# Optimization experiments

Measured on AMD Instinct MI355X. Metric: run time of the kernel, lower is better.

The kernel has to match this reference:

```python
import jax, jax.numpy as jnp
import numpy as np

B, S, F_IN, F_OUT = 8, 128, 768, 768
NUM_REL = 41           # num_dependencies + 1
NUM_LAYER = 2
N_HEAD, HID = 8, 96    # hidden_dim = embed_dim // n_head
EMB = 768


def setup_inputs() -> dict:
    key = jax.random.key(0)
    ks = jax.random.split(key, 14)
    s = 1.0 / np.sqrt(F_IN)
    inp = {
        "x": jax.random.normal(ks[0], (B, S, F_IN), dtype=jnp.float32),
        "adj": jax.random.uniform(ks[1], (B, NUM_REL, S, S), dtype=jnp.float32),
        "q": jax.random.normal(ks[2], (B, EMB), dtype=jnp.float32),
        # R-GCN params (stacked over layers)
        "w_rgcn": jax.random.uniform(ks[3], (NUM_LAYER, NUM_REL, F_IN, F_OUT), minval=-s, maxval=s),
        "score_w": jax.random.uniform(ks[4], (NUM_LAYER, F_OUT), minval=-s, maxval=s),
        "score_b": jax.random.uniform(ks[5], (NUM_LAYER,), minval=-s, maxval=s),
        # Attention params (stored as [in, out] for x @ W)
        "wk": jax.random.uniform(ks[6], (EMB, N_HEAD * HID), minval=-s, maxval=s),
        "bk": jnp.zeros((N_HEAD * HID,), jnp.float32),
        "wq": jax.random.uniform(ks[7], (EMB, N_HEAD * HID), minval=-s, maxval=s),
        "bq": jnp.zeros((N_HEAD * HID,), jnp.float32),
        "wbil": jax.random.uniform(ks[8], (HID, HID), minval=-1.0 / np.sqrt(HID), maxval=1.0 / np.sqrt(HID)),
        "wproj": jax.random.uniform(ks[9], (N_HEAD * HID, EMB), minval=-s, maxval=s),
        "bproj": jnp.zeros((EMB,), jnp.float32),
    }
    return inp


def _rgcn_layer(h, adj, w, sw, sb):
    # h: [B,S,I]; adj: [B,R,S,S]; w: [R,I,O]
    hidden = jnp.einsum("bsi,rio->brso", h, w)            # per-relation transform
    denom = jnp.sum(adj, axis=3, keepdims=True)           # [B,R,S,1]
    intm = jnp.einsum("brsk,brko->brso", adj, hidden)     # relation-wise aggregation
    div = intm / jnp.where(denom == 0, jnp.ones_like(denom), denom)
    logits = jnp.einsum("brso,o->brs", div, sw) + sb      # score Linear(out->1)
    r_coeffs = jax.nn.softmax(logits, axis=1)             # softmax over relations
    out = jnp.einsum("brso,brs->bso", div, r_coeffs)
    return jax.nn.relu(out)


def _attention(k, q, wk, bk, wq, bq, wbil, wproj, bproj):
    # k: [B,S,E]; q: [B,E] -> [B,1,E]
    q3 = q[:, None, :]
    kx = (k @ wk + bk).reshape(B, S, N_HEAD, HID)
    qx = (q3 @ wq + bq).reshape(B, 1, N_HEAD, HID)
    qw = jnp.einsum("bqhd,de->bqhe", qx, wbil)            # bi_linear score
    score = jnp.einsum("bqhe,bkhe->bhqk", qw, kx)
    attn = jax.nn.softmax(score, axis=-1)
    o = jnp.einsum("bhqk,bkhd->bqhd", attn, kx).reshape(B, 1, N_HEAD * HID)
    return o @ wproj + bproj                              # [B,1,EMB]


def reference(x, adj, q, w_rgcn, score_w, score_b, wk, bk, wq, bq, wbil, wproj, bproj):
    h = x
    for l in range(NUM_LAYER):
        h = _rgcn_layer(h, adj, w_rgcn[l], score_w[l], score_b[l])
    return _attention(h, q, wk, bk, wq, bq, wbil, wproj, bproj)
```

## Files before the change

### kernel.cpp

```cpp
#include <hip/hip_runtime.h>
#include <stdint.h>

#define B_ 8
#define S_ 128
#define R_ 41
#define F_ 768
#define NH_ 8
#define HID_ 96
#define BS_ (B_*S_)
#define SM_SCALE 256.0f

typedef _Float16 f16;
typedef _Float16 f16x8 __attribute__((ext_vector_type(8)));
typedef _Float16 f16x4 __attribute__((ext_vector_type(4)));
typedef float f32x4 __attribute__((ext_vector_type(4)));

#define GLD16(gp, lp) __builtin_amdgcn_global_load_lds((const __attribute__((address_space(1))) uint32_t*)(gp), (__attribute__((address_space(3))) uint32_t*)(lp), 16, 0, 0)

__device__ __forceinline__ float wredsum(float v){
  #pragma unroll
  for (int o=32;o;o>>=1) v += __shfl_down(v,o,64);
  return v;
}

__global__ __launch_bounds__(256) void kConvWV(const float* __restrict__ w, const float* __restrict__ sw,
                                               f16* __restrict__ wT, float* __restrict__ v) {
  int bid = blockIdx.x;
  int it = bid % 12, r = bid / 12;
  __shared__ float t[64*68];
  int tid = threadIdx.x;
  int ri = tid >> 2, c = tid & 3;
  float vacc = 0.f;
  for (int ot = 0; ot < 12; ++ot) {
    const float* src = w + ((size_t)r*F_ + (it*64 + ri))*F_ + ot*64 + c*16;
    const float* swp = sw + ot*64 + c*16;
    __syncthreads();
    #pragma unroll
    for (int j=0;j<4;j++){
      f32x4 v4 = *(const f32x4*)(src + j*4);
      f32x4 s4 = *(const f32x4*)(swp + j*4);
      vacc += v4.x*s4.x + v4.y*s4.y + v4.z*s4.z + v4.w*s4.w;
      *(f32x4*)&t[ri*68 + c*16 + j*4] = v4;
    }
    __syncthreads();
    int ro = tid >> 2;
    f16 outv[16];
    #pragma unroll
    for (int j=0;j<16;j++) outv[j] = (f16)t[(c*16+j)*68 + ro];
    f16* dst = wT + ((size_t)r*F_ + (ot*64+ro))*F_ + it*64 + c*16;
    *(f16x8*)dst = *(f16x8*)&outv[0];
    *(f16x8*)(dst+8) = *(f16x8*)&outv[8];
  }
  vacc += __shfl_down(vacc, 1, 64);
  vacc += __shfl_down(vacc, 2, 64);
  if (c == 0) v[(size_t)r*F_ + it*64 + ri] = vacc;
}

__global__ __launch_bounds__(256) void kConvW(const float* __restrict__ w, f16* __restrict__ wT) {
  int bid = blockIdx.x;
  int ot = bid % 12; int it = (bid/12) % 12; int r = bid / 144;
  __shared__ float t[64*68];
  int tid = threadIdx.x;
  int ri = tid >> 2, c = tid & 3;
  const float* src = w + ((size_t)r*F_ + (it*64 + ri))*F_ + ot*64 + c*16;
  #pragma unroll
  for (int j=0;j<4;j++){
    f32x4 v4 = *(const f32x4*)(src + j*4);
    *(f32x4*)&t[ri*68 + c*16 + j*4] = v4;
  }
  __syncthreads();
  int ro = tid >> 2;
  f16 outv[16];
  #pragma unroll
  for (int j=0;j<16;j++) outv[j] = (f16)t[(c*16+j)*68 + ro];
  f16* dst = wT + ((size_t)r*F_ + (ot*64+ro))*F_ + it*64 + c*16;
  *(f16x8*)dst = *(f16x8*)&outv[0];
  *(f16x8*)(dst+8) = *(f16x8*)&outv[8];
}

template<typename T>
__global__ __launch_bounds__(256) void kTransTo16T(const T* __restrict__ h, f16* __restrict__ hT) {
  int bid = blockIdx.x;
  int st = bid & 1; int ft = (bid>>1) % 12; int b = bid / 24;
  __shared__ f16 t[64*72];
  int tid = threadIdx.x;
  int sl = tid>>2, c = tid&3;
  const T* src = h + ((size_t)b*S_ + st*64 + sl)*F_ + ft*64 + c*16;
  f16 tmp[16];
  #pragma unroll
  for (int j=0;j<16;j++) tmp[j] = (f16)src[j];
  *(f16x8*)&t[sl*72 + c*16]     = *(f16x8*)&tmp[0];
  *(f16x8*)&t[sl*72 + c*16 + 8] = *(f16x8*)&tmp[8];
  __syncthreads();
  int fl = tid>>2;
  f16 outv[16];
  #pragma unroll
  for (int j=0;j<16;j++) outv[j] = t[(c*16+j)*72 + fl];
  f16* dst = hT + ((size_t)b*F_ + ft*64 + fl)*S_ + st*64 + c*16;
  *(f16x8*)dst = *(f16x8*)&outv[0];
  *(f16x8*)(dst+8) = *(f16x8*)&outv[8];
}

__global__ __launch_bounds__(256) void kU(const float* __restrict__ h, const float* __restrict__ v, float* __restrict__ u) {
  int idx = blockIdx.x*4 + (threadIdx.x>>6);
  int lane = threadIdx.x&63;
  int k = idx & 127;
  int br = idx >> 7;
  int r = br % R_;
  int b = br / R_;
  const float* hr = h + ((size_t)b*S_ + k)*F_ + lane*12;
  const float* vr = v + (size_t)r*F_ + lane*12;
  float acc=0.f;
  #pragma unroll
  for (int j=0;j<3;j++){
    f32x4 a = *(const f32x4*)(hr+j*4);
    f32x4 c4 = *(const f32x4*)(vr+j*4);
    acc += a.x*c4.x+a.y*c4.y+a.z*c4.z+a.w*c4.w;
  }
  acc = wredsum(acc);
  if (lane==0) u[idx] = acc;
}

__global__ __launch_bounds__(256) void kLogits(const float* __restrict__ adj, const float* __restrict__ u,
                        const float* __restrict__ sb_all, int l,
                        float* __restrict__ dinv, float* __restrict__ lg) {
  int idx = blockIdx.x*4 + (threadIdx.x>>6);
  int lane = threadIdx.x&63;
  const float* arow = adj + (size_t)idx*S_;
  int br = idx >> 7;
  const float* up = u + (size_t)br*S_;
  float a0 = arow[lane], a1 = arow[lane+64];
  float u0 = up[lane],   u1 = up[lane+64];
  float ssum = a0+a1;
  float sdot = a0*u0 + a1*u1;
  ssum = wredsum(ssum);
  sdot = wredsum(sdot);
  if (lane==0){
    float dv = (ssum==0.0f) ? 1.0f : (1.0f/ssum);
    dinv[idx] = dv;
    lg[idx] = sdot*dv + sb_all[l];
  }
}

__global__ __launch_bounds__(256) void kSoftmaxR(const float* __restrict__ lg, float* __restrict__ c) {
  int t = blockIdx.x*256 + threadIdx.x;
  int b = t >> 7, s = t & 127;
  float vals[R_];
  float mx = -1e30f;
  #pragma unroll
  for (int r=0;r<R_;r++){ float x = lg[((size_t)b*R_+r)*S_ + s]; vals[r]=x; mx = fmaxf(mx,x); }
  float sum=0.f;
  #pragma unroll
  for (int r=0;r<R_;r++){ vals[r] = expf(vals[r]-mx); sum += vals[r]; }
  float inv = 1.0f/sum;
  #pragma unroll
  for (int r=0;r<R_;r++) c[((size_t)b*R_+r)*S_+s] = vals[r]*inv;
}

__global__ __launch_bounds__(256) void kM16(const float* __restrict__ adj, const float* __restrict__ c,
                     const float* __restrict__ dinv, f16* __restrict__ M) {
  int t = blockIdx.x*256 + threadIdx.x;
  int brs = t >> 5; int k4 = (t & 31) * 4;
  float a = SM_SCALE * c[brs] * dinv[brs];
  f32x4 v4 = *(const f32x4*)(adj + (size_t)brs*S_ + k4);
  f16x4 o;
  o[0]=(f16)(v4.x*a); o[1]=(f16)(v4.y*a); o[2]=(f16)(v4.z*a); o[3]=(f16)(v4.w*a);
  *(f16x4*)(M + (size_t)brs*S_ + k4) = o;
}

__global__ __launch_bounds__(256) void kGgemm(const f16* __restrict__ M, const f16* __restrict__ hT, f16* __restrict__ G) {
  __shared__ f16 lds[2*16384];
  f16* lsA = lds;
  f16* lsB = lds + 16384;
  int bid = blockIdx.x;
  int nt = bid % 6; int r = (bid/6) % R_; int b = bid/(6*R_);
  int tid = threadIdx.x, wid = tid>>6, lane = tid&63;
  const f16* Ab = M + (size_t)(b*R_ + r)*(S_*S_);
  const f16* Bb = hT + ((size_t)b*F_ + nt*128)*S_;
  #pragma unroll
  for (int j=0;j<8;j++){
    int qd = wid*8 + j;
    GLD16(Ab + qd*512 + lane*8, lsA + qd*512);
    GLD16(Bb + qd*512 + lane*8, lsB + qd*512);
  }
  __syncthreads();
  f32x4 acc[4][4] = {};
  int wr = wid>>1, wc = wid&1;
  int lr = lane&15, kk0 = (lane>>4)*8;
  #pragma unroll
  for (int ks=0;ks<4;ks++){
    int kk = ks*32 + kk0;
    f16x8 av[4], bv[4];
    #pragma unroll
    for (int i=0;i<4;i++) av[i] = *(const f16x8*)&lsA[(wr*64+i*16+lr)*128 + kk];
    #pragma unroll
    for (int i=0;i<4;i++) bv[i] = *(const f16x8*)&lsB[(wc*64+i*16+lr)*128 + kk];
    #pragma unroll
    for (int mi=0;mi<4;mi++)
      #pragma unroll
      for (int ni=0;ni<4;ni++)
        acc[mi][ni] = __builtin_amdgcn_mfma_f32_16x16x32_f16(av[mi],bv[ni],acc[mi][ni],0,0,0);
  }
  __syncthreads();
  #pragma unroll
  for (int mi=0;mi<4;mi++)
    #pragma unroll
    for (int ni=0;ni<4;ni++){
      int row = wr*64 + mi*16 + (lane>>4)*4;
      int col = wc*64 + ni*16 + lr;
      #pragma unroll
      for (int i=0;i<4;i++)
        lds[(row+i)*136 + col] = (f16)acc[mi][ni][i];
    }
  __syncthreads();
  int row = tid>>1, seg = tid&1;
  f16* dst = G + ((size_t)(b*R_ + r)*S_ + row)*F_ + nt*128 + seg*64;
  const f16* sl = lds + row*136 + seg*64;
  #pragma unroll
  for (int j=0;j<8;j++) *(f16x8*)(dst + j*8) = *(const f16x8*)(sl + j*8);
}

__global__ __launch_bounds__(256) void kOutGemm(const f16* __restrict__ G, const f16* __restrict__ WT, float* __restrict__ Cp) {
  __shared__ f16 lsA[128*64];
  __shared__ f16 lsB[128*64];
  int bid = blockIdx.x;
  int nt = bid % 6, g = (bid/6) % 12, mt = bid/72;
  int r0 = (g<5)? g*4 : 20 + (g-5)*3;
  int nr = (g<5)? 4 : 3;
  int tid = threadIdx.x, wid = tid>>6, lane = tid&63;
  size_t abase[4], bbase[4];
  #pragma unroll
  for (int j=0;j<4;j++){
    int qd = wid*4 + j;
    int row = mt*128 + qd*8 + (lane>>3);
    int b = row >> 7, s = row & 127;
    abase[j] = ((size_t)b*R_*S_ + s)*F_ + (lane&7)*8;
    int o = nt*128 + qd*8 + (lane>>3);
    bbase[j] = (size_t)o*F_ + (lane&7)*8;
  }
  f32x4 acc[4][4] = {};
  int wr = wid>>1, wc = wid&1;
  int lr = lane&15, kk0 = (lane>>4)*8;
  for (int rr=0; rr<nr; ++rr){
    int r = r0 + rr;
    const f16* Ar = G  + (size_t)r*S_*F_;
    const f16* Br = WT + (size_t)r*F_*F_;
    for (int it=0; it<12; ++it){
      #pragma unroll
      for (int j=0;j<4;j++){
        int qd = wid*4+j;
        GLD16(Ar + abase[j] + it*64, lsA + qd*512);
        GLD16(Br + bbase[j] + it*64, lsB + qd*512);
      }
      __syncthreads();
      #pragma unroll
      for (int ks=0;ks<2;ks++){
        int kk = ks*32 + kk0;
        f16x8 av[4], bv[4];
        #pragma unroll
        for (int i=0;i<4;i++) av[i] = *(const f16x8*)&lsA[(wr*64+i*16+lr)*64 + kk];
        #pragma unroll
        for (int i=0;i<4;i++) bv[i] = *(const f16x8*)&lsB[(wc*64+i*16+lr)*64 + kk];
        #pragma unroll
        for (int mi=0;mi<4;mi++)
          #pragma unroll
          for (int ni=0;ni<4;ni++)
            acc[mi][ni] = __builtin_amdgcn_mfma_f32_16x16x32_f16(av[mi],bv[ni],acc[mi][ni],0,0,0);
      }
      __syncthreads();
    }
  }
  #pragma unroll
  for (int mi=0;mi<4;mi++)
    #pragma unroll
    for (int ni=0;ni<4;ni++){
      int row = mt*128 + wr*64 + mi*16 + (lane>>4)*4;
      int col = nt*128 + wc*64 + ni*16 + lr;
      #pragma unroll
      for (int i=0;i<4;i++)
        Cp[((size_t)g*BS_ + row + i)*F_ + col] = acc[mi][ni][i];
    }
}

__global__ __launch_bounds__(256) void kReduce(const float* __restrict__ Cp, float* __restrict__ h32, f16* __restrict__ h16o) {
  int t = blockIdx.x*256 + threadIdx.x;
  size_t i4 = (size_t)t*4;
  f32x4 s = {};
  #pragma unroll
  for (int g=0; g<12; g++){
    f32x4 v4 = *(const f32x4*)(Cp + (size_t)g*BS_*F_ + i4);
    s.x += v4.x; s.y += v4.y; s.z += v4.z; s.w += v4.w;
  }
  const float inv = 1.0f/SM_SCALE;
  f32x4 rr;
  rr.x = fmaxf(s.x*inv, 0.f); rr.y = fmaxf(s.y*inv, 0.f);
  rr.z = fmaxf(s.z*inv, 0.f); rr.w = fmaxf(s.w*inv, 0.f);
  *(f32x4*)(h32 + i4) = rr;
  f16x4 o; o[0]=(f16)rr.x; o[1]=(f16)rr.y; o[2]=(f16)rr.z; o[3]=(f16)rr.w;
  *(f16x4*)(h16o + i4) = o;
}

__global__ __launch_bounds__(256) void kKx(const f16* __restrict__ A, const f16* __restrict__ BT,
                    const float* __restrict__ bias, float* __restrict__ C) {
  __shared__ f16 lsA[128*64];
  __shared__ f16 lsB[128*64];
  int bid = blockIdx.x;
  int nt = bid % 6, mt = bid / 6;
  int tid = threadIdx.x, wid = tid>>6, lane = tid&63;
  size_t abase[4], bbase[4];
  #pragma unroll
  for (int j=0;j<4;j++){
    int qd = wid*4 + j;
    int row = mt*128 + qd*8 + (lane>>3);
    abase[j] = (size_t)row*F_ + (lane&7)*8;
    int o = nt*128 + qd*8 + (lane>>3);
    bbase[j] = (size_t)o*F_ + (lane&7)*8;
  }
  f32x4 acc[4][4] = {};
  int wr = wid>>1, wc = wid&1;
  int lr = lane&15, kk0 = (lane>>4)*8;
  for (int it=0; it<12; ++it){
    #pragma unroll
    for (int j=0;j<4;j++){
      int qd = wid*4+j;
      GLD16(A + abase[j] + it*64, lsA + qd*512);
      GLD16(BT + bbase[j] + it*64, lsB + qd*512);
    }
    __syncthreads();
    #pragma unroll
    for (int ks=0;ks<2;ks++){
      int kk = ks*32 + kk0;
      f16x8 av[4], bv[4];
      #pragma unroll
      for (int i=0;i<4;i++) av[i] = *(const f16x8*)&lsA[(wr*64+i*16+lr)*64 + kk];
      #pragma unroll
      for (int i=0;i<4;i++) bv[i] = *(const f16x8*)&lsB[(wc*64+i*16+lr)*64 + kk];
      #pragma unroll
      for (int mi=0;mi<4;mi++)
        #pragma unroll
        for (int ni=0;ni<4;ni++)
          acc[mi][ni] = __builtin_amdgcn_mfma_f32_16x16x32_f16(av[mi],bv[ni],acc[mi][ni],0,0,0);
    }
    __syncthreads();
  }
  #pragma unroll
  for (int mi=0;mi<4;mi++)
    #pragma unroll
    for (int ni=0;ni<4;ni++){
      int row = mt*128 + wr*64 + mi*16 + (lane>>4)*4;
      int col = nt*128 + wc*64 + ni*16 + lr;
      float bb = bias[col];
      #pragma unroll
      for (int i=0;i<4;i++)
        C[(size_t)(row+i)*F_ + col] = acc[mi][ni][i] + bb;
    }
}

__global__ __launch_bounds__(256) void kAttn(const float* __restrict__ kx, const float* __restrict__ qin,
                      const float* __restrict__ wq, const float* __restrict__ bq,
                      const float* __restrict__ wbil, float* __restrict__ obuf) {
  int bid = blockIdx.x; int h = bid & 7; int b = bid >> 3;
  __shared__ float qx[HID_], qw[HID_], sc[S_];
  __shared__ float smax, ssum;
  int t = threadIdx.x;
  if (t < HID_) {
    float a0=0.f,a1=0.f,a2=0.f,a3=0.f;
    const float* qp = qin + (size_t)b*F_;
    const float* wp = wq + h*HID_ + t;
    for (int i=0;i<F_;i+=4){
      a0 += qp[i]*wp[(size_t)i*F_];
      a1 += qp[i+1]*wp[(size_t)(i+1)*F_];
      a2 += qp[i+2]*wp[(size_t)(i+2)*F_];
      a3 += qp[i+3]*wp[(size_t)(i+3)*F_];
    }
    qx[t] = a0+a1+a2+a3 + bq[h*HID_+t];
  }
  __syncthreads();
  if (t < HID_) {
    float a0=0.f,a1=0.f;
    for (int e=0;e<HID_;e+=2){ a0 += qx[e]*wbil[e*HID_+t]; a1 += qx[e+1]*wbil[(e+1)*HID_+t]; }
    qw[t] = a0+a1;
  }
  __syncthreads();
  if (t < S_) {
    float a0=0.f,a1=0.f;
    const float* kp = kx + ((size_t)b*S_ + t)*F_ + h*HID_;
    for (int e=0;e<HID_;e+=2){ a0 += qw[e]*kp[e]; a1 += qw[e+1]*kp[e+1]; }
    sc[t] = a0+a1;
  }
  __syncthreads();
  if (t < 64) {
    float m = fmaxf(sc[t], sc[t+64]);
    #pragma unroll
    for (int o=32;o;o>>=1) m = fmaxf(m, __shfl_down(m,o,64));
    if (t==0) smax = m;
  }
  __syncthreads();
  if (t < S_) sc[t] = expf(sc[t]-smax);
  __syncthreads();
  if (t < 64) {
    float s = sc[t] + sc[t+64];
    s = wredsum(s);
    if (t==0) ssum = s;
  }
  __syncthreads();
  if (t < HID_) {
    float a0=0.f,a1=0.f;
    const float* kp = kx + ((size_t)b*S_)*F_ + h*HID_ + t;
    for (int k=0;k<S_;k+=2){ a0 += sc[k]*kp[(size_t)k*F_]; a1 += sc[k+1]*kp[(size_t)(k+1)*F_]; }
    obuf[(size_t)b*F_ + h*HID_ + t] = (a0+a1)/ssum;
  }
}

__global__ __launch_bounds__(256) void kProj(const float* __restrict__ obuf, const float* __restrict__ wproj,
                      const float* __restrict__ bproj, float* __restrict__ outp) {
  int bid = blockIdx.x; int b = bid/3, seg = bid%3;
  int t = threadIdx.x;
  __shared__ float ov[F_];
  for (int j=t;j<F_;j+=256) ov[j] = obuf[(size_t)b*F_ + j];
  __syncthreads();
  int col = seg*256 + t;
  float a0=0.f,a1=0.f,a2=0.f,a3=0.f;
  for (int j=0;j<F_;j+=4){
    a0 += ov[j]*wproj[(size_t)j*F_+col];
    a1 += ov[j+1]*wproj[(size_t)(j+1)*F_+col];
    a2 += ov[j+2]*wproj[(size_t)(j+2)*F_+col];
    a3 += ov[j+3]*wproj[(size_t)(j+3)*F_+col];
  }
  outp[(size_t)b*F_ + col] = bproj[col] + a0+a1+a2+a3;
}

extern "C" void kernel_launch(void* const* d_in, const int* in_sizes, int n_in,
                              void* d_out, int out_size, void* d_ws, size_t ws_size,
                              hipStream_t stream) {
  (void)in_sizes; (void)n_in; (void)out_size;
  const float* x      = (const float*)d_in[0];
  const float* adj    = (const float*)d_in[1];
  const float* qin    = (const float*)d_in[2];
  const float* w_rgcn = (const float*)d_in[3];
  const float* score_w= (const float*)d_in[4];
  const float* score_b= (const float*)d_in[5];
  const float* wk     = (const float*)d_in[6];
  const float* bk     = (const float*)d_in[7];
  const float* wq     = (const float*)d_in[8];
  const float* bq     = (const float*)d_in[9];
  const float* wbil   = (const float*)d_in[10];
  const float* wproj  = (const float*)d_in[11];
  const float* bproj  = (const float*)d_in[12];
  float* outp = (float*)d_out;

  char* p = (char*)d_ws;
  auto alloc = [&](size_t bytes)->char* {
    char* r = p; p += (bytes + 255) & ~(size_t)255; return r;
  };
  f16*   w16T  = (f16*)  alloc((size_t)R_*F_*F_*2);
  f16*   G16   = (f16*)  alloc((size_t)B_*R_*S_*F_*2);
  f16*   M16   = (f16*)  alloc((size_t)B_*R_*S_*S_*2);
  float* Cpart = (float*)alloc((size_t)12*BS_*F_*4);
  float* h32a  = (float*)alloc((size_t)BS_*F_*4);
  float* h32b  = (float*)alloc((size_t)BS_*F_*4);
  f16*   h16row= (f16*)  alloc((size_t)BS_*F_*2);
  f16*   h16T  = (f16*)  alloc((size_t)BS_*F_*2);
  float* kx    = (float*)alloc((size_t)BS_*F_*4);
  f16*   wkT   = (f16*)  alloc((size_t)F_*F_*2);
  float* vbuf  = (float*)alloc((size_t)R_*F_*4);
  float* ubuf  = (float*)alloc((size_t)B_*R_*S_*4);
  float* dinv  = (float*)alloc((size_t)B_*R_*S_*4);
  float* lgb   = (float*)alloc((size_t)B_*R_*S_*4);
  float* cbuf  = (float*)alloc((size_t)B_*R_*S_*4);
  float* obuf  = (float*)alloc((size_t)B_*F_*4);
  if ((size_t)(p - (char*)d_ws) > ws_size) return;

  const size_t WL = (size_t)R_*F_*F_;

  kConvWV<<<R_*12, 256, 0, stream>>>(w_rgcn, score_w, w16T, vbuf);
  kTransTo16T<float><<<192, 256, 0, stream>>>(x, h16T);
  kU<<<10496, 256, 0, stream>>>(x, vbuf, ubuf);
  kLogits<<<10496, 256, 0, stream>>>(adj, ubuf, score_b, 0, dinv, lgb);
  kSoftmaxR<<<4, 256, 0, stream>>>(lgb, cbuf);
  kM16<<<5248, 256, 0, stream>>>(adj, cbuf, dinv, M16);
  kGgemm<<<B_*R_*6, 256, 0, stream>>>(M16, h16T, G16);
  kOutGemm<<<576, 256, 0, stream>>>(G16, w16T, Cpart);
  kReduce<<<768, 256, 0, stream>>>(Cpart, h32a, h16row);
  kTransTo16T<f16><<<192, 256, 0, stream>>>(h16row, h16T);

  kConvWV<<<R_*12, 256, 0, stream>>>(w_rgcn + WL, score_w + F_, w16T, vbuf);
  kU<<<10496, 256, 0, stream>>>(h32a, vbuf, ubuf);
  kLogits<<<10496, 256, 0, stream>>>(adj, ubuf, score_b, 1, dinv, lgb);
  kSoftmaxR<<<4, 256, 0, stream>>>(lgb, cbuf);
  kM16<<<5248, 256, 0, stream>>>(adj, cbuf, dinv, M16);
  kGgemm<<<B_*R_*6, 256, 0, stream>>>(M16, h16T, G16);
  kOutGemm<<<576, 256, 0, stream>>>(G16, w16T, Cpart);
  kReduce<<<768, 256, 0, stream>>>(Cpart, h32b, h16row);

  kConvW<<<144, 256, 0, stream>>>(wk, wkT);
  kKx<<<48, 256, 0, stream>>>(h16row, wkT, bk, kx);
  kAttn<<<64, 256, 0, stream>>>(kx, qin, wq, bq, wbil, obuf);
  kProj<<<24, 256, 0, stream>>>(obuf, wproj, bproj, outp);
}
```

Before: 530.4 us.

## Enlarge output GEMM tile to 256x256 with 512 threads and finer relation split-K

Reworks the relation-summed output GEMM to use 256x256 tiles computed by 8 waves of 512-thread blocks, each wave holding a 128x64 accumulator. The relation split-K changes from 12 groups of 3-4 relations to 21 groups of 2 relations (the last holding one), giving 252 blocks. Larger tiles raise arithmetic intensity and cut redundant loads of the G and W operands. The cost is more partial-sum traffic: 21 fp32 partial buffers are written and then read by the reduce kernel, plus higher register pressure and a single-relation tail group.

Measured after the change: 514.0 us. 1.03x faster.

```diff
diff --git a/kernel.cpp b/kernel.cpp
--- a/kernel.cpp
+++ b/kernel.cpp
@@ -9,6 +9,7 @@
 #define HID_ 96
 #define BS_ (B_*S_)
 #define SM_SCALE 256.0f
+#define NG_ 21
 
 typedef _Float16 f16;
 typedef _Float16 f16x8 __attribute__((ext_vector_type(8)));
@@ -220,26 +221,27 @@
   for (int j=0;j<8;j++) *(f16x8*)(dst + j*8) = *(const f16x8*)(sl + j*8);
 }
 
-__global__ __launch_bounds__(256) void kOutGemm(const f16* __restrict__ G, const f16* __restrict__ WT, float* __restrict__ Cp) {
-  __shared__ f16 lsA[128*64];
-  __shared__ f16 lsB[128*64];
+__global__ __launch_bounds__(512,2) void kOutGemm(const f16* __restrict__ G, const f16* __restrict__ WT, float* __restrict__ Cp) {
+  __shared__ f16 lsA[256*64];
+  __shared__ f16 lsB[256*64];
   int bid = blockIdx.x;
-  int nt = bid % 6, g = (bid/6) % 12, mt = bid/72;
-  int r0 = (g<5)? g*4 : 20 + (g-5)*3;
-  int nr = (g<5)? 4 : 3;
+  int t12 = bid % 12, g = bid / 12;
+  int nt = t12 % 3, mt = t12 / 3;
+  int r0 = (g<20)? 2*g : 40;
+  int nr = (g<20)? 2 : 1;
   int tid = threadIdx.x, wid = tid>>6, lane = tid&63;
   size_t abase[4], bbase[4];
   #pragma unroll
   for (int j=0;j<4;j++){
-    int qd = wid*4 + j;
-    int row = mt*128 + qd*8 + (lane>>3);
-    int b = row >> 7, s = row & 127;
-    abase[j] = ((size_t)b*R_*S_ + s)*F_ + (lane&7)*8;
-    int o = nt*128 + qd*8 + (lane>>3);
-    bbase[j] = (size_t)o*F_ + (lane&7)*8;
-  }
-  f32x4 acc[4][4] = {};
-  int wr = wid>>1, wc = wid&1;
+    int chunk = wid*4 + j;
+    int arow = mt*256 + chunk*8 + (lane>>3);
+    int b = arow >> 7, s = arow & 127;
+    abase[j] = ((size_t)b*R_*S_ + s)*(size_t)F_ + (lane&7)*8;
+    int orow = nt*256 + chunk*8 + (lane>>3);
+    bbase[j] = (size_t)orow*F_ + (lane&7)*8;
+  }
+  f32x4 acc[8][4] = {};
+  int wr = wid>>2, wc = wid&3;
   int lr = lane&15, kk0 = (lane>>4)*8;
   for (int rr=0; rr<nr; ++rr){
     int r = r0 + rr;
@@ -248,21 +250,21 @@
     for (int it=0; it<12; ++it){
       #pragma unroll
       for (int j=0;j<4;j++){
-        int qd = wid*4+j;
-        GLD16(Ar + abase[j] + it*64, lsA + qd*512);
-        GLD16(Br + bbase[j] + it*64, lsB + qd*512);
+        int chunk = wid*4 + j;
+        GLD16(Ar + abase[j] + it*64, lsA + chunk*512);
+        GLD16(Br + bbase[j] + it*64, lsB + chunk*512);
       }
       __syncthreads();
       #pragma unroll
       for (int ks=0;ks<2;ks++){
         int kk = ks*32 + kk0;
-        f16x8 av[4], bv[4];
+        f16x8 av[8], bv[4];
         #pragma unroll
-        for (int i=0;i<4;i++) av[i] = *(const f16x8*)&lsA[(wr*64+i*16+lr)*64 + kk];
+        for (int i=0;i<8;i++) av[i] = *(const f16x8*)&lsA[(wr*128+i*16+lr)*64 + kk];
         #pragma unroll
         for (int i=0;i<4;i++) bv[i] = *(const f16x8*)&lsB[(wc*64+i*16+lr)*64 + kk];
         #pragma unroll
-        for (int mi=0;mi<4;mi++)
+        for (int mi=0;mi<8;mi++)
           #pragma unroll
           for (int ni=0;ni<4;ni++)
             acc[mi][ni] = __builtin_amdgcn_mfma_f32_16x16x32_f16(av[mi],bv[ni],acc[mi][ni],0,0,0);
@@ -271,11 +273,11 @@
     }
   }
   #pragma unroll
-  for (int mi=0;mi<4;mi++)
+  for (int mi=0;mi<8;mi++)
     #pragma unroll
     for (int ni=0;ni<4;ni++){
-      int row = mt*128 + wr*64 + mi*16 + (lane>>4)*4;
-      int col = nt*128 + wc*64 + ni*16 + lr;
+      int row = mt*256 + wr*128 + mi*16 + (lane>>4)*4;
+      int col = nt*256 + wc*64 + ni*16 + lr;
       #pragma unroll
       for (int i=0;i<4;i++)
         Cp[((size_t)g*BS_ + row + i)*F_ + col] = acc[mi][ni][i];
@@ -287,7 +289,7 @@
   size_t i4 = (size_t)t*4;
   f32x4 s = {};
   #pragma unroll
-  for (int g=0; g<12; g++){
+  for (int g=0; g<NG_; g++){
     f32x4 v4 = *(const f32x4*)(Cp + (size_t)g*BS_*F_ + i4);
     s.x += v4.x; s.y += v4.y; s.z += v4.z; s.w += v4.w;
   }
@@ -456,7 +458,7 @@
   f16*   w16T  = (f16*)  alloc((size_t)R_*F_*F_*2);
   f16*   G16   = (f16*)  alloc((size_t)B_*R_*S_*F_*2);
   f16*   M16   = (f16*)  alloc((size_t)B_*R_*S_*S_*2);
-  float* Cpart = (float*)alloc((size_t)12*BS_*F_*4);
+  float* Cpart = (float*)alloc((size_t)NG_*BS_*F_*4);
   float* h32a  = (float*)alloc((size_t)BS_*F_*4);
   float* h32b  = (float*)alloc((size_t)BS_*F_*4);
   f16*   h16row= (f16*)  alloc((size_t)BS_*F_*2);
@@ -480,7 +482,7 @@
   kSoftmaxR<<<4, 256, 0, stream>>>(lgb, cbuf);
   kM16<<<5248, 256, 0, stream>>>(adj, cbuf, dinv, M16);
   kGgemm<<<B_*R_*6, 256, 0, stream>>>(M16, h16T, G16);
-  kOutGemm<<<576, 256, 0, stream>>>(G16, w16T, Cpart);
+  kOutGemm<<<12*NG_, 512, 0, stream>>>(G16, w16T, Cpart);
   kReduce<<<768, 256, 0, stream>>>(Cpart, h32a, h16row);
   kTransTo16T<f16><<<192, 256, 0, stream>>>(h16row, h16T);
 
@@ -490,7 +492,7 @@
   kSoftmaxR<<<4, 256, 0, stream>>>(lgb, cbuf);
   kM16<<<5248, 256, 0, stream>>>(adj, cbuf, dinv, M16);
   kGgemm<<<B_*R_*6, 256, 0, stream>>>(M16, h16T, G16);
-  kOutGemm<<<576, 256, 0, stream>>>(G16, w16T, Cpart);
+  kOutGemm<<<12*NG_, 512, 0, stream>>>(G16, w16T, Cpart);
   kReduce<<<768, 256, 0, stream>>>(Cpart, h32b, h16row);
 
   kConvW<<<144, 256, 0, stream>>>(wk, wkT);
```
